# Performance work log

Hardware: AMD Instinct MI355X
Metric: run time of the kernel (lower is better)

The kernel has to match this reference:

```python
import jax, jax.numpy as jnp
import numpy as np

DIM = 1024
NUM_EXPERTS = 8
ACTIVE_EXPERTS = 2
EXPERT_DIM = 2048


def setup_inputs() -> dict:
    key = jax.random.key(0)
    k1, k2, k3, k4 = jax.random.split(key, 4)
    x = jax.random.normal(k1, (1, 2048, DIM), dtype=jnp.float32)
    gate_w = jax.random.normal(k2, (NUM_EXPERTS, DIM), dtype=jnp.float32) * 0.02
    balance_bias = jnp.zeros((NUM_EXPERTS,), dtype=jnp.float32)
    w1 = jax.random.normal(k3, (NUM_EXPERTS, EXPERT_DIM, DIM), dtype=jnp.float32) * 0.02
    w2 = jax.random.normal(k4, (NUM_EXPERTS, DIM, EXPERT_DIM), dtype=jnp.float32) * 0.02
    return {"x": x, "gate_w": gate_w, "balance_bias": balance_bias, "w1": w1, "w2": w2}


def reference(x, gate_w, balance_bias, w1, w2):
    B, S, D = x.shape
    T = B * S
    xf = x.reshape(T, D)
    # gating: sigmoid scores with load-balance bias, then top-k
    gate_logits = jnp.einsum('td,ed->te', xf, gate_w)
    gate_scores = jax.nn.sigmoid(gate_logits + balance_bias)
    topk_scores, topk_idx = jax.lax.top_k(gate_scores, ACTIVE_EXPERTS)
    topk_scores = topk_scores / (topk_scores.sum(axis=-1, keepdims=True) + 1e-6)
    # scatter normalized scores into dense combine weights [T, E]
    comb = jnp.zeros((T, NUM_EXPERTS), dtype=x.dtype)
    comb = comb.at[jnp.arange(T)[:, None], topk_idx].add(topk_scores)
    # expert FFNs (dense over experts; combine weight zeroes unselected)
    h = jax.nn.silu(jnp.einsum('td,ehd->teh', xf, w1))   # [T, E, expert_dim]
    expert_out = jnp.einsum('teh,edh->ted', h, w2)        # [T, E, D]
    out = jnp.einsum('te,ted->td', comb, expert_out)
    return out.reshape(B, S, D)
```

## Files before the change

### kernel.cpp

```cpp
#include <hip/hip_runtime.h>

#define T 2048
#define DIM 1024
#define NE 8
#define ED 2048
#define NSLOT (T * 2)
#define KSPLIT 2

#define BM 128
#define BN 128
#define BK 32
#define MAXWL 40

typedef __attribute__((ext_vector_type(8))) short s8v;
typedef __attribute__((ext_vector_type(4))) float f32x4;

__device__ __forceinline__ short f2bf(float f) {
    union { float f; unsigned u; } v;
    v.f = f;
    unsigned r = 0x7FFFu + ((v.u >> 16) & 1u);
    v.u += r;
    return (short)(v.u >> 16);
}

__device__ __forceinline__ float bf2f(short s) {
    union { unsigned u; float f; } v;
    v.u = ((unsigned)(unsigned short)s) << 16;
    return v.f;
}

__device__ __forceinline__ unsigned pkbf2(float lo, float hi) {
    union { float f; unsigned u; } a, b;
    a.f = lo; b.f = hi;
    return __builtin_amdgcn_perm(b.u + 0x8000u, a.u + 0x8000u, 0x07060302u);
}

__device__ __forceinline__ void glds16(const void* g, void* l) {
    __builtin_amdgcn_global_load_lds(
        (const __attribute__((address_space(1))) void*)g,
        (__attribute__((address_space(3))) void*)l, 16, 0, 0);
}

__global__ __launch_bounds__(256) void convert_kernel(const float* __restrict__ src,
                                                      short* __restrict__ dst, int n8) {
    int stride = gridDim.x * 256;
    for (int i = blockIdx.x * 256 + threadIdx.x; i < n8; i += stride) {
        float4 a = ((const float4*)src)[2 * i];
        float4 b = ((const float4*)src)[2 * i + 1];
        uint4 o = { pkbf2(a.x, a.y), pkbf2(a.z, a.w), pkbf2(b.x, b.y), pkbf2(b.z, b.w) };
        ((uint4*)dst)[i] = o;
    }
}

__global__ void router_kernel(const float* __restrict__ x,
                              const float* __restrict__ gw,
                              const float* __restrict__ bias,
                              short* __restrict__ xb,
                              int* __restrict__ counts,
                              int* __restrict__ top2i,
                              float* __restrict__ top2w) {
    int wid = threadIdx.x >> 6;
    int lane = threadIdx.x & 63;
    int t = blockIdx.x * 4 + wid;

    const float* xr = x + (size_t)t * DIM + lane * 16;
    float4 xv[4];
#pragma unroll
    for (int j = 0; j < 4; ++j) xv[j] = *(const float4*)(xr + j * 4);

    s8v o0, o1;
#pragma unroll
    for (int j = 0; j < 2; ++j) {
        o0[j * 4 + 0] = f2bf(xv[j].x); o0[j * 4 + 1] = f2bf(xv[j].y);
        o0[j * 4 + 2] = f2bf(xv[j].z); o0[j * 4 + 3] = f2bf(xv[j].w);
        o1[j * 4 + 0] = f2bf(xv[j + 2].x); o1[j * 4 + 1] = f2bf(xv[j + 2].y);
        o1[j * 4 + 2] = f2bf(xv[j + 2].z); o1[j * 4 + 3] = f2bf(xv[j + 2].w);
    }
    *(s8v*)(xb + (size_t)t * DIM + lane * 16) = o0;
    *(s8v*)(xb + (size_t)t * DIM + lane * 16 + 8) = o1;

    float sc[NE];
#pragma unroll
    for (int e = 0; e < NE; ++e) {
        const float* gr = gw + e * DIM + lane * 16;
        float p = 0.f;
#pragma unroll
        for (int j = 0; j < 4; ++j) {
            float4 g = *(const float4*)(gr + j * 4);
            p += xv[j].x * g.x + xv[j].y * g.y + xv[j].z * g.z + xv[j].w * g.w;
        }
#pragma unroll
        for (int off = 32; off; off >>= 1) p += __shfl_xor(p, off, 64);
        sc[e] = 1.f / (1.f + __expf(-(p + bias[e])));
    }
    int b0 = 0; float s0 = sc[0];
#pragma unroll
    for (int e = 1; e < NE; ++e) if (sc[e] > s0) { s0 = sc[e]; b0 = e; }
    int b1 = -1; float s1 = -1e30f;
#pragma unroll
    for (int e = 0; e < NE; ++e) if (e != b0 && sc[e] > s1) { s1 = sc[e]; b1 = e; }
    float inv = 1.f / (s0 + s1 + 1e-6f);
    if (lane == 0) {
        top2i[t * 2 + 0] = b0; top2i[t * 2 + 1] = b1;
        top2w[t * 2 + 0] = s0 * inv; top2w[t * 2 + 1] = s1 * inv;
        atomicAdd(&counts[b0], 1);
        atomicAdd(&counts[b1], 1);
    }
}

__global__ __launch_bounds__(256) void plan_kernel(
    const int* __restrict__ counts, const int* __restrict__ top2i,
    int* __restrict__ offsets, int* __restrict__ tok_list, int* __restrict__ slot_of,
    int* __restrict__ wl, int* __restrict__ nwl) {
    __shared__ int soff[NE];
    __shared__ int srun[NE];
    if (threadIdx.x == 0) {
        int a = 0;
        for (int e = 0; e < NE; ++e) { soff[e] = a; offsets[e] = a; a += counts[e]; srun[e] = 0; }
        int n = 0;
        for (int e = 0; e < NE; ++e) {
            int mt = (counts[e] + BM - 1) / BM;
            for (int m = 0; m < mt; ++m) wl[n++] = (e << 16) | m;
        }
        *nwl = n;
    }
    __syncthreads();
    for (int t = threadIdx.x; t < T; t += 256) {
#pragma unroll
        for (int k = 0; k < 2; ++k) {
            int e = top2i[t * 2 + k];
            int pos = atomicAdd(&srun[e], 1);
            int slot = soff[e] + pos;
            tok_list[slot] = t;
            slot_of[t * 2 + k] = slot;
        }
    }
}

template <int BF>
__global__ __launch_bounds__(256) void ffn1_kernel(
    const short* __restrict__ xb, const float* __restrict__ w1,
    const short* __restrict__ wb,
    const int* __restrict__ counts, const int* __restrict__ offsets,
    const int* __restrict__ tok_list, const int* __restrict__ wl,
    const int* __restrict__ nwl, short* __restrict__ h) {
    int my = blockIdx.y;
    if (my >= *nwl) return;
    int e = wl[my] >> 16;
    int m0 = (wl[my] & 0xffff) * BM;
    int cnt = counts[e];
    int off = offsets[e];
    int n0 = blockIdx.x * BN;

    __shared__ __align__(16) short As[2][4][BM][8];
    __shared__ __align__(16) short Bs[2][4][BN][8];

    int tid = threadIdx.x;
    int lane = tid & 63, w = tid >> 6;
    int mo = (w >> 1) * 64, no = (w & 1) * 64;
    int lrow = lane & 15, lq = lane >> 4;

    f32x4 acc[4][4];
#pragma unroll
    for (int mi = 0; mi < 4; ++mi)
#pragma unroll
        for (int ni = 0; ni < 4; ++ni) acc[mi][ni] = (f32x4){0.f, 0.f, 0.f, 0.f};

    int ra0 = m0 + lane;      if (ra0 > cnt - 1) ra0 = cnt - 1;
    int ra1 = m0 + 64 + lane; if (ra1 > cnt - 1) ra1 = cnt - 1;
    const short* a0 = xb + (size_t)tok_list[off + ra0] * DIM + w * 8;
    const short* a1 = xb + (size_t)tok_list[off + ra1] * DIM + w * 8;

    const short* b0 = wb + ((size_t)e * ED + n0 + (w & 1) * 64 + lane) * DIM + (w >> 1) * 8;
    int br = tid >> 1, bq = tid & 1;
    const float* bp = w1 + ((size_t)e * ED + n0 + br) * DIM + bq * 16;

    const int NK = DIM / BK;
    float4 L0, L1, L2, L3;

    glds16(a0, &As[0][w][0][0]);
    glds16(a1, &As[0][w][64][0]);
    if constexpr (BF) {
        glds16(b0, &Bs[0][w >> 1][(w & 1) * 64][0]);
        glds16(b0 + 16, &Bs[0][2 + (w >> 1)][(w & 1) * 64][0]);
    } else {
        L0 = *(const float4*)(bp);     L1 = *(const float4*)(bp + 4);
        L2 = *(const float4*)(bp + 8); L3 = *(const float4*)(bp + 12);
        {
            uint4 p0 = { pkbf2(L0.x, L0.y), pkbf2(L0.z, L0.w), pkbf2(L1.x, L1.y), pkbf2(L1.z, L1.w) };
            uint4 p1 = { pkbf2(L2.x, L2.y), pkbf2(L2.z, L2.w), pkbf2(L3.x, L3.y), pkbf2(L3.z, L3.w) };
            *(uint4*)&Bs[0][2 * bq][br][0] = p0;
            *(uint4*)&Bs[0][2 * bq + 1][br][0] = p1;
        }
        L0 = *(const float4*)(bp + BK);     L1 = *(const float4*)(bp + BK + 4);
        L2 = *(const float4*)(bp + BK + 8); L3 = *(const float4*)(bp + BK + 12);
    }

    for (int kk = 0; kk < NK; ++kk) {
        int cur = kk & 1, nxt = cur ^ 1;
        __syncthreads();
        if (kk + 1 < NK) {
            int k0 = (kk + 1) * BK;
            glds16(a0 + k0, &As[nxt][w][0][0]);
            glds16(a1 + k0, &As[nxt][w][64][0]);
            if constexpr (BF) {
                glds16(b0 + k0, &Bs[nxt][w >> 1][(w & 1) * 64][0]);
                glds16(b0 + k0 + 16, &Bs[nxt][2 + (w >> 1)][(w & 1) * 64][0]);
            } else {
                uint4 p0 = { pkbf2(L0.x, L0.y), pkbf2(L0.z, L0.w), pkbf2(L1.x, L1.y), pkbf2(L1.z, L1.w) };
                uint4 p1 = { pkbf2(L2.x, L2.y), pkbf2(L2.z, L2.w), pkbf2(L3.x, L3.y), pkbf2(L3.z, L3.w) };
                *(uint4*)&Bs[nxt][2 * bq][br][0] = p0;
                *(uint4*)&Bs[nxt][2 * bq + 1][br][0] = p1;
                if (kk + 2 < NK) {
                    const float* bpp = bp + (kk + 2) * BK;
                    L0 = *(const float4*)(bpp);     L1 = *(const float4*)(bpp + 4);
                    L2 = *(const float4*)(bpp + 8); L3 = *(const float4*)(bpp + 12);
                }
            }
        }
        s8v af[4], bfr[4];
#pragma unroll
        for (int mi = 0; mi < 4; ++mi) af[mi] = *(const s8v*)&As[cur][lq][mo + mi * 16 + lrow][0];
#pragma unroll
        for (int ni = 0; ni < 4; ++ni) bfr[ni] = *(const s8v*)&Bs[cur][lq][no + ni * 16 + lrow][0];
#pragma unroll
        for (int mi = 0; mi < 4; ++mi)
#pragma unroll
            for (int ni = 0; ni < 4; ++ni)
                acc[mi][ni] = __builtin_amdgcn_mfma_f32_16x16x32_bf16(af[mi], bfr[ni], acc[mi][ni], 0, 0, 0);
    }

#pragma unroll
    for (int mi = 0; mi < 4; ++mi) {
#pragma unroll
        for (int ni = 0; ni < 4; ++ni) {
            int ln = n0 + no + ni * 16 + lrow;
#pragma unroll
            for (int r = 0; r < 4; ++r) {
                int row = m0 + mo + mi * 16 + lq * 4 + r;
                if (row < cnt) {
                    float v = acc[mi][ni][r];
                    v = v / (1.f + __expf(-v));
                    h[(size_t)(off + row) * ED + ln] = f2bf(v);
                }
            }
        }
    }
}

template <int BF>
__global__ __launch_bounds__(256) void ffn2_kernel(
    const short* __restrict__ h, const float* __restrict__ w2,
    const short* __restrict__ wb,
    const int* __restrict__ counts, const int* __restrict__ offsets,
    const int* __restrict__ wl, const int* __restrict__ nwl,
    short* __restrict__ eo) {
    int my = blockIdx.y;
    if (my >= *nwl) return;
    int e = wl[my] >> 16;
    int m0 = (wl[my] & 0xffff) * BM;
    int ksp = blockIdx.z;
    int cnt = counts[e];
    int off = offsets[e];
    int n0 = blockIdx.x * BN;
    const int kbase = ksp * (ED / KSPLIT);

    __shared__ __align__(16) short As[2][4][BM][8];
    __shared__ __align__(16) short Bs[2][4][BN][8];

    int tid = threadIdx.x;
    int lane = tid & 63, w = tid >> 6;
    int mo = (w >> 1) * 64, no = (w & 1) * 64;
    int lrow = lane & 15, lq = lane >> 4;

    f32x4 acc[4][4];
#pragma unroll
    for (int mi = 0; mi < 4; ++mi)
#pragma unroll
        for (int ni = 0; ni < 4; ++ni) acc[mi][ni] = (f32x4){0.f, 0.f, 0.f, 0.f};

    int ra0 = m0 + lane;      if (ra0 > cnt - 1) ra0 = cnt - 1;
    int ra1 = m0 + 64 + lane; if (ra1 > cnt - 1) ra1 = cnt - 1;
    const short* a0 = h + (size_t)(off + ra0) * ED + kbase + w * 8;
    const short* a1 = h + (size_t)(off + ra1) * ED + kbase + w * 8;

    const short* b0 = wb + ((size_t)e * DIM + n0 + (w & 1) * 64 + lane) * ED + kbase + (w >> 1) * 8;
    int br = tid >> 1, bq = tid & 1;
    const float* bp = w2 + ((size_t)e * DIM + n0 + br) * ED + kbase + bq * 16;

    const int NK = (ED / KSPLIT) / BK;
    float4 L0, L1, L2, L3;

    glds16(a0, &As[0][w][0][0]);
    glds16(a1, &As[0][w][64][0]);
    if constexpr (BF) {
        glds16(b0, &Bs[0][w >> 1][(w & 1) * 64][0]);
        glds16(b0 + 16, &Bs[0][2 + (w >> 1)][(w & 1) * 64][0]);
    } else {
        L0 = *(const float4*)(bp);     L1 = *(const float4*)(bp + 4);
        L2 = *(const float4*)(bp + 8); L3 = *(const float4*)(bp + 12);
        {
            uint4 p0 = { pkbf2(L0.x, L0.y), pkbf2(L0.z, L0.w), pkbf2(L1.x, L1.y), pkbf2(L1.z, L1.w) };
            uint4 p1 = { pkbf2(L2.x, L2.y), pkbf2(L2.z, L2.w), pkbf2(L3.x, L3.y), pkbf2(L3.z, L3.w) };
            *(uint4*)&Bs[0][2 * bq][br][0] = p0;
            *(uint4*)&Bs[0][2 * bq + 1][br][0] = p1;
        }
        L0 = *(const float4*)(bp + BK);     L1 = *(const float4*)(bp + BK + 4);
        L2 = *(const float4*)(bp + BK + 8); L3 = *(const float4*)(bp + BK + 12);
    }

    for (int kk = 0; kk < NK; ++kk) {
        int cur = kk & 1, nxt = cur ^ 1;
        __syncthreads();
        if (kk + 1 < NK) {
            int k0 = (kk + 1) * BK;
            glds16(a0 + k0, &As[nxt][w][0][0]);
            glds16(a1 + k0, &As[nxt][w][64][0]);
            if constexpr (BF) {
                glds16(b0 + k0, &Bs[nxt][w >> 1][(w & 1) * 64][0]);
                glds16(b0 + k0 + 16, &Bs[nxt][2 + (w >> 1)][(w & 1) * 64][0]);
            } else {
                uint4 p0 = { pkbf2(L0.x, L0.y), pkbf2(L0.z, L0.w), pkbf2(L1.x, L1.y), pkbf2(L1.z, L1.w) };
                uint4 p1 = { pkbf2(L2.x, L2.y), pkbf2(L2.z, L2.w), pkbf2(L3.x, L3.y), pkbf2(L3.z, L3.w) };
                *(uint4*)&Bs[nxt][2 * bq][br][0] = p0;
                *(uint4*)&Bs[nxt][2 * bq + 1][br][0] = p1;
                if (kk + 2 < NK) {
                    const float* bpp = bp + (kk + 2) * BK;
                    L0 = *(const float4*)(bpp);     L1 = *(const float4*)(bpp + 4);
                    L2 = *(const float4*)(bpp + 8); L3 = *(const float4*)(bpp + 12);
                }
            }
        }
        s8v af[4], bfr[4];
#pragma unroll
        for (int mi = 0; mi < 4; ++mi) af[mi] = *(const s8v*)&As[cur][lq][mo + mi * 16 + lrow][0];
#pragma unroll
        for (int ni = 0; ni < 4; ++ni) bfr[ni] = *(const s8v*)&Bs[cur][lq][no + ni * 16 + lrow][0];
#pragma unroll
        for (int mi = 0; mi < 4; ++mi)
#pragma unroll
            for (int ni = 0; ni < 4; ++ni)
                acc[mi][ni] = __builtin_amdgcn_mfma_f32_16x16x32_bf16(af[mi], bfr[ni], acc[mi][ni], 0, 0, 0);
    }

    short* eop = eo + (size_t)ksp * NSLOT * DIM;
#pragma unroll
    for (int mi = 0; mi < 4; ++mi) {
#pragma unroll
        for (int ni = 0; ni < 4; ++ni) {
            int ln = n0 + no + ni * 16 + lrow;
#pragma unroll
            for (int r = 0; r < 4; ++r) {
                int row = m0 + mo + mi * 16 + lq * 4 + r;
                if (row < cnt) {
                    eop[(size_t)(off + row) * DIM + ln] = f2bf(acc[mi][ni][r]);
                }
            }
        }
    }
}

__global__ __launch_bounds__(256) void combine_kernel(
    const short* __restrict__ eo, const int* __restrict__ slot_of,
    const float* __restrict__ top2w, float* __restrict__ out) {
    int idx = blockIdx.x * 256 + threadIdx.x;
    int t = idx >> 7;
    int c = idx & 127;
    int s0 = slot_of[2 * t], s1 = slot_of[2 * t + 1];
    float w0 = top2w[2 * t], w1 = top2w[2 * t + 1];
    const short* e0 = eo;
    const short* e1 = eo + (size_t)NSLOT * DIM;
    s8v a0 = *(const s8v*)(e0 + (size_t)s0 * DIM + c * 8);
    s8v a1 = *(const s8v*)(e1 + (size_t)s0 * DIM + c * 8);
    s8v b0 = *(const s8v*)(e0 + (size_t)s1 * DIM + c * 8);
    s8v b1 = *(const s8v*)(e1 + (size_t)s1 * DIM + c * 8);
    float4 o[2];
#pragma unroll
    for (int j = 0; j < 8; ++j) {
        float v = w0 * (bf2f(a0[j]) + bf2f(a1[j])) + w1 * (bf2f(b0[j]) + bf2f(b1[j]));
        ((float*)o)[j] = v;
    }
    float4* op = (float4*)(out + (size_t)t * DIM + c * 8);
    op[0] = o[0];
    op[1] = o[1];
}

extern "C" void kernel_launch(void* const* d_in, const int* in_sizes, int n_in,
                              void* d_out, int out_size, void* d_ws, size_t ws_size,
                              hipStream_t stream) {
    const float* x    = (const float*)d_in[0];
    const float* gw   = (const float*)d_in[1];
    const float* bias = (const float*)d_in[2];
    const float* w1   = (const float*)d_in[3];
    const float* w2   = (const float*)d_in[4];
    float* out = (float*)d_out;

    char* ws = (char*)d_ws;
    short* xb = (short*)ws;
    short* h  = (short*)(ws + (4ull << 20));
    short* eo = (short*)(ws + (20ull << 20));
    char* meta = ws + (36ull << 20);
    int*   counts   = (int*)(meta);
    int*   offsets  = (int*)(meta + 64);
    int*   tok_list = (int*)(meta + 128);
    int*   slot_of  = (int*)(meta + 128 + 4 * NSLOT);
    int*   top2i    = (int*)(meta + 128 + 8 * NSLOT);
    float* top2w    = (float*)(meta + 128 + 8 * NSLOT + 8 * T);
    int*   wl       = (int*)(meta + 128 + 8 * NSLOT + 16 * T);
    int*   nwl      = (int*)(meta + 128 + 8 * NSLOT + 16 * T + 4 * MAXWL);
    short* wb       = (short*)(ws + (37ull << 20));

    bool bf = ws_size >= (70ull << 20);

    hipMemsetAsync(counts, 0, 32, stream);

    if (bf) {
        convert_kernel<<<2048, 256, 0, stream>>>(w1, wb, NE * ED * DIM / 8);
    }
    router_kernel<<<T / 4, 256, 0, stream>>>(x, gw, bias, xb, counts, top2i, top2w);
    plan_kernel<<<1, 256, 0, stream>>>(counts, top2i, offsets, tok_list, slot_of, wl, nwl);
    if (bf) {
        ffn1_kernel<1><<<dim3(ED / BN, MAXWL), 256, 0, stream>>>(xb, w1, wb, counts, offsets, tok_list, wl, nwl, h);
        convert_kernel<<<2048, 256, 0, stream>>>(w2, wb, NE * DIM * ED / 8);
        ffn2_kernel<1><<<dim3(DIM / BN, MAXWL, KSPLIT), 256, 0, stream>>>(h, w2, wb, counts, offsets, wl, nwl, eo);
    } else {
        ffn1_kernel<0><<<dim3(ED / BN, MAXWL), 256, 0, stream>>>(xb, w1, nullptr, counts, offsets, tok_list, wl, nwl, h);
        ffn2_kernel<0><<<dim3(DIM / BN, MAXWL, KSPLIT), 256, 0, stream>>>(h, w2, nullptr, counts, offsets, wl, nwl, eo);
    }
    combine_kernel<<<T * DIM / 8 / 256, 256, 0, stream>>>(eo, slot_of, top2w, out);
}
```

Before: 345.1 us.

## Deepen bf16-weight GEMM pipeline to four LDS stages with vmcnt-based waits

For the pre-converted bf16 weight path in both FFN kernels, the shared-memory buffers grow from two to four stages and three k-tiles are prefetched ahead. A plain __syncthreads is replaced with an explicit s_waitcnt vmcnt(8) plus s_barrier, so the loads for upcoming tiles stay in flight while the current tile is consumed. The aim is to hide global-to-LDS latency. In exchange, LDS use doubles, which can lower occupancy, and correctness now depends on the hand-written vmcnt count. Tail iterations keep issuing redundant loads of the last tile.

```diff
diff --git a/kernel.cpp b/kernel.cpp
--- a/kernel.cpp
+++ b/kernel.cpp
@@ -152,8 +152,8 @@
     int off = offsets[e];
     int n0 = blockIdx.x * BN;
 
-    __shared__ __align__(16) short As[2][4][BM][8];
-    __shared__ __align__(16) short Bs[2][4][BN][8];
+    __shared__ __align__(16) short As[BF ? 4 : 2][4][BM][8];
+    __shared__ __align__(16) short Bs[BF ? 4 : 2][4][BN][8];
 
     int tid = threadIdx.x;
     int lane = tid & 63, w = tid >> 6;
@@ -176,14 +176,36 @@
     const float* bp = w1 + ((size_t)e * ED + n0 + br) * DIM + bq * 16;
 
     const int NK = DIM / BK;
-    float4 L0, L1, L2, L3;
-
-    glds16(a0, &As[0][w][0][0]);
-    glds16(a1, &As[0][w][64][0]);
+
     if constexpr (BF) {
-        glds16(b0, &Bs[0][w >> 1][(w & 1) * 64][0]);
-        glds16(b0 + 16, &Bs[0][2 + (w >> 1)][(w & 1) * 64][0]);
+        auto stage = [&](int s, int b) {
+            int k0 = s * BK;
+            glds16(a0 + k0, &As[b][w][0][0]);
+            glds16(a1 + k0, &As[b][w][64][0]);
+            glds16(b0 + k0, &Bs[b][w >> 1][(w & 1) * 64][0]);
+            glds16(b0 + k0 + 16, &Bs[b][2 + (w >> 1)][(w & 1) * 64][0]);
+        };
+        stage(0, 0); stage(1, 1); stage(2, 2);
+        for (int kk = 0; kk < NK; ++kk) {
+            asm volatile("s_waitcnt vmcnt(8)\n\ts_barrier" ::: "memory");
+            int cur = kk & 3;
+            int s = kk + 3 < NK ? kk + 3 : NK - 1;
+            stage(s, (kk + 3) & 3);
+            s8v af[4], bfr[4];
+#pragma unroll
+            for (int mi = 0; mi < 4; ++mi) af[mi] = *(const s8v*)&As[cur][lq][mo + mi * 16 + lrow][0];
+#pragma unroll
+            for (int ni = 0; ni < 4; ++ni) bfr[ni] = *(const s8v*)&Bs[cur][lq][no + ni * 16 + lrow][0];
+#pragma unroll
+            for (int mi = 0; mi < 4; ++mi)
+#pragma unroll
+                for (int ni = 0; ni < 4; ++ni)
+                    acc[mi][ni] = __builtin_amdgcn_mfma_f32_16x16x32_bf16(af[mi], bfr[ni], acc[mi][ni], 0, 0, 0);
+        }
     } else {
+        float4 L0, L1, L2, L3;
+        glds16(a0, &As[0][w][0][0]);
+        glds16(a1, &As[0][w][64][0]);
         L0 = *(const float4*)(bp);     L1 = *(const float4*)(bp + 4);
         L2 = *(const float4*)(bp + 8); L3 = *(const float4*)(bp + 12);
         {
@@ -194,19 +216,13 @@
         }
         L0 = *(const float4*)(bp + BK);     L1 = *(const float4*)(bp + BK + 4);
         L2 = *(const float4*)(bp + BK + 8); L3 = *(const float4*)(bp + BK + 12);
-    }
-
-    for (int kk = 0; kk < NK; ++kk) {
-        int cur = kk & 1, nxt = cur ^ 1;
-        __syncthreads();
-        if (kk + 1 < NK) {
-            int k0 = (kk + 1) * BK;
-            glds16(a0 + k0, &As[nxt][w][0][0]);
-            glds16(a1 + k0, &As[nxt][w][64][0]);
-            if constexpr (BF) {
-                glds16(b0 + k0, &Bs[nxt][w >> 1][(w & 1) * 64][0]);
-                glds16(b0 + k0 + 16, &Bs[nxt][2 + (w >> 1)][(w & 1) * 64][0]);
-            } else {
+        for (int kk = 0; kk < NK; ++kk) {
+            int cur = kk & 1, nxt = cur ^ 1;
+            __syncthreads();
+            if (kk + 1 < NK) {
+                int k0 = (kk + 1) * BK;
+                glds16(a0 + k0, &As[nxt][w][0][0]);
+                glds16(a1 + k0, &As[nxt][w][64][0]);
                 uint4 p0 = { pkbf2(L0.x, L0.y), pkbf2(L0.z, L0.w), pkbf2(L1.x, L1.y), pkbf2(L1.z, L1.w) };
                 uint4 p1 = { pkbf2(L2.x, L2.y), pkbf2(L2.z, L2.w), pkbf2(L3.x, L3.y), pkbf2(L3.z, L3.w) };
                 *(uint4*)&Bs[nxt][2 * bq][br][0] = p0;
@@ -217,17 +233,17 @@
                     L2 = *(const float4*)(bpp + 8); L3 = *(const float4*)(bpp + 12);
                 }
             }
-        }
-        s8v af[4], bfr[4];
-#pragma unroll
-        for (int mi = 0; mi < 4; ++mi) af[mi] = *(const s8v*)&As[cur][lq][mo + mi * 16 + lrow][0];
-#pragma unroll
-        for (int ni = 0; ni < 4; ++ni) bfr[ni] = *(const s8v*)&Bs[cur][lq][no + ni * 16 + lrow][0];
-#pragma unroll
-        for (int mi = 0; mi < 4; ++mi)
-#pragma unroll
-            for (int ni = 0; ni < 4; ++ni)
-                acc[mi][ni] = __builtin_amdgcn_mfma_f32_16x16x32_bf16(af[mi], bfr[ni], acc[mi][ni], 0, 0, 0);
+            s8v af[4], bfr[4];
+#pragma unroll
+            for (int mi = 0; mi < 4; ++mi) af[mi] = *(const s8v*)&As[cur][lq][mo + mi * 16 + lrow][0];
+#pragma unroll
+            for (int ni = 0; ni < 4; ++ni) bfr[ni] = *(const s8v*)&Bs[cur][lq][no + ni * 16 + lrow][0];
+#pragma unroll
+            for (int mi = 0; mi < 4; ++mi)
+#pragma unroll
+                for (int ni = 0; ni < 4; ++ni)
+                    acc[mi][ni] = __builtin_amdgcn_mfma_f32_16x16x32_bf16(af[mi], bfr[ni], acc[mi][ni], 0, 0, 0);
+        }
     }
 
 #pragma unroll
@@ -265,8 +281,8 @@
     int n0 = blockIdx.x * BN;
     const int kbase = ksp * (ED / KSPLIT);
 
-    __shared__ __align__(16) short As[2][4][BM][8];
-    __shared__ __align__(16) short Bs[2][4][BN][8];
+    __shared__ __align__(16) short As[BF ? 4 : 2][4][BM][8];
+    __shared__ __align__(16) short Bs[BF ? 4 : 2][4][BN][8];
 
     int tid = threadIdx.x;
     int lane = tid & 63, w = tid >> 6;
@@ -289,14 +305,36 @@
     const float* bp = w2 + ((size_t)e * DIM + n0 + br) * ED + kbase + bq * 16;
 
     const int NK = (ED / KSPLIT) / BK;
-    float4 L0, L1, L2, L3;
-
-    glds16(a0, &As[0][w][0][0]);
-    glds16(a1, &As[0][w][64][0]);
+
     if constexpr (BF) {
-        glds16(b0, &Bs[0][w >> 1][(w & 1) * 64][0]);
-        glds16(b0 + 16, &Bs[0][2 + (w >> 1)][(w & 1) * 64][0]);
+        auto stage = [&](int s, int b) {
+            int k0 = s * BK;
+            glds16(a0 + k0, &As[b][w][0][0]);
+            glds16(a1 + k0, &As[b][w][64][0]);
+            glds16(b0 + k0, &Bs[b][w >> 1][(w & 1) * 64][0]);
+            glds16(b0 + k0 + 16, &Bs[b][2 + (w >> 1)][(w & 1) * 64][0]);
+        };
+        stage(0, 0); stage(1, 1); stage(2, 2);
+        for (int kk = 0; kk < NK; ++kk) {
+            asm volatile("s_waitcnt vmcnt(8)\n\ts_barrier" ::: "memory");
+            int cur = kk & 3;
+            int s = kk + 3 < NK ? kk + 3 : NK - 1;
+            stage(s, (kk + 3) & 3);
+            s8v af[4], bfr[4];
+#pragma unroll
+            for (int mi = 0; mi < 4; ++mi) af[mi] = *(const s8v*)&As[cur][lq][mo + mi * 16 + lrow][0];
+#pragma unroll
+            for (int ni = 0; ni < 4; ++ni) bfr[ni] = *(const s8v*)&Bs[cur][lq][no + ni * 16 + lrow][0];
+#pragma unroll
+            for (int mi = 0; mi < 4; ++mi)
+#pragma unroll
+                for (int ni = 0; ni < 4; ++ni)
+                    acc[mi][ni] = __builtin_amdgcn_mfma_f32_16x16x32_bf16(af[mi], bfr[ni], acc[mi][ni], 0, 0, 0);
+        }
     } else {
+        float4 L0, L1, L2, L3;
+        glds16(a0, &As[0][w][0][0]);
+        glds16(a1, &As[0][w][64][0]);
         L0 = *(const float4*)(bp);     L1 = *(const float4*)(bp + 4);
         L2 = *(const float4*)(bp + 8); L3 = *(const float4*)(bp + 12);
         {
@@ -307,19 +345,13 @@
         }
         L0 = *(const float4*)(bp + BK);     L1 = *(const float4*)(bp + BK + 4);
         L2 = *(const float4*)(bp + BK + 8); L3 = *(const float4*)(bp + BK + 12);
-    }
-
-    for (int kk = 0; kk < NK; ++kk) {
-        int cur = kk & 1, nxt = cur ^ 1;
-        __syncthreads();
-        if (kk + 1 < NK) {
-            int k0 = (kk + 1) * BK;
-            glds16(a0 + k0, &As[nxt][w][0][0]);
-            glds16(a1 + k0, &As[nxt][w][64][0]);
-            if constexpr (BF) {
-                glds16(b0 + k0, &Bs[nxt][w >> 1][(w & 1) * 64][0]);
-                glds16(b0 + k0 + 16, &Bs[nxt][2 + (w >> 1)][(w & 1) * 64][0]);
-            } else {
+        for (int kk = 0; kk < NK; ++kk) {
+            int cur = kk & 1, nxt = cur ^ 1;
+            __syncthreads();
+            if (kk + 1 < NK) {
+                int k0 = (kk + 1) * BK;
+                glds16(a0 + k0, &As[nxt][w][0][0]);
+                glds16(a1 + k0, &As[nxt][w][64][0]);
                 uint4 p0 = { pkbf2(L0.x, L0.y), pkbf2(L0.z, L0.w), pkbf2(L1.x, L1.y), pkbf2(L1.z, L1.w) };
                 uint4 p1 = { pkbf2(L2.x, L2.y), pkbf2(L2.z, L2.w), pkbf2(L3.x, L3.y), pkbf2(L3.z, L3.w) };
                 *(uint4*)&Bs[nxt][2 * bq][br][0] = p0;
@@ -330,17 +362,17 @@
                     L2 = *(const float4*)(bpp + 8); L3 = *(const float4*)(bpp + 12);
                 }
             }
-        }
-        s8v af[4], bfr[4];
-#pragma unroll
-        for (int mi = 0; mi < 4; ++mi) af[mi] = *(const s8v*)&As[cur][lq][mo + mi * 16 + lrow][0];
-#pragma unroll
-        for (int ni = 0; ni < 4; ++ni) bfr[ni] = *(const s8v*)&Bs[cur][lq][no + ni * 16 + lrow][0];
-#pragma unroll
-        for (int mi = 0; mi < 4; ++mi)
-#pragma unroll
-            for (int ni = 0; ni < 4; ++ni)
-                acc[mi][ni] = __builtin_amdgcn_mfma_f32_16x16x32_bf16(af[mi], bfr[ni], acc[mi][ni], 0, 0, 0);
+            s8v af[4], bfr[4];
+#pragma unroll
+            for (int mi = 0; mi < 4; ++mi) af[mi] = *(const s8v*)&As[cur][lq][mo + mi * 16 + lrow][0];
+#pragma unroll
+            for (int ni = 0; ni < 4; ++ni) bfr[ni] = *(const s8v*)&Bs[cur][lq][no + ni * 16 + lrow][0];
+#pragma unroll
+            for (int mi = 0; mi < 4; ++mi)
+#pragma unroll
+                for (int ni = 0; ni < 4; ++ni)
+                    acc[mi][ni] = __builtin_amdgcn_mfma_f32_16x16x32_bf16(af[mi], bfr[ni], acc[mi][ni], 0, 0, 0);
+        }
     }
 
     short* eop = eo + (size_t)ksp * NSLOT * DIM;
```

Result: slower. 387.0 us (+12.1%).
